# Optimization experiments

Measured on AMD Instinct MI355X. Metric: run time of the kernel, lower is better.

Reference implementation:

```python
import jax, jax.numpy as jnp
import numpy as np

C_IN = 1024
N_HEADS = 16
C_HEAD = C_IN // N_HEADS  # 64
ROPE_BASE = 10000.0


def setup_inputs() -> dict:
    key = jax.random.key(0)
    ks = jax.random.split(key, 7)
    B, S = 2, 2048
    q = jax.random.normal(ks[0], (B, S, C_IN), dtype=jnp.float32)
    k = jax.random.normal(ks[1], (B, S, C_IN), dtype=jnp.float32)
    v = jax.random.normal(ks[2], (B, S, C_IN), dtype=jnp.float32)
    # nn.Linear weights [out, in], y = x @ W.T (no bias)
    sc = 1.0 / np.sqrt(C_IN)
    Wq = jax.random.uniform(ks[3], (C_IN, C_IN), jnp.float32, -sc, sc)
    Wk = jax.random.uniform(ks[4], (C_IN, C_IN), jnp.float32, -sc, sc)
    Wv = jax.random.uniform(ks[5], (C_IN, C_IN), jnp.float32, -sc, sc)
    Wo = jax.random.uniform(ks[6], (C_IN, C_IN), jnp.float32, -sc, sc)
    return {"q": q, "k": k, "v": v, "Wq": Wq, "Wk": Wk, "Wv": Wv, "Wo": Wo}


def _rope_tables(S, dtype):
    inv_freq = 1.0 / (ROPE_BASE ** (jnp.arange(0, C_HEAD, 2, dtype=jnp.float32) / C_HEAD))
    t = jnp.arange(S, dtype=jnp.float32)
    freqs = jnp.einsum('i,j->ij', t, inv_freq)          # [S, C_HEAD/2]
    emb = jnp.concatenate([freqs, freqs], axis=-1)      # [S, C_HEAD]
    cos = jnp.cos(emb)[None, None, :, :].astype(dtype)  # [1,1,S,D]
    sin = jnp.sin(emb)[None, None, :, :].astype(dtype)
    return cos, sin


def _rotate_half(x):
    x1, x2 = jnp.split(x, 2, axis=-1)
    return jnp.concatenate([-x2, x1], axis=-1)


def reference(q, k, v, Wq, Wk, Wv, Wo):
    B, S, _ = q.shape
    # QKV projections, reshape to [B, H, S, D]
    def proj(x, W):
        return (x @ W.T).reshape(B, -1, N_HEADS, C_HEAD).transpose(0, 2, 1, 3)
    qh, kh, vh = proj(q, Wq), proj(k, Wk), proj(v, Wv)
    # rotary embedding
    cos, sin = _rope_tables(S, qh.dtype)
    qh = qh * cos + _rotate_half(qh) * sin
    kh = kh * cos + _rotate_half(kh) * sin
    # scaled dot-product attention (no mask, dropout p=0)
    scale = 1.0 / np.sqrt(C_HEAD)
    scores = jnp.einsum('bhqd,bhkd->bhqk', qh, kh) * scale
    attn = jax.nn.softmax(scores, axis=-1)              # [B,H,S,S]
    out = jnp.einsum('bhqk,bhkd->bhqd', attn, vh)
    out = out.transpose(0, 2, 1, 3).reshape(B, S, N_HEADS * C_HEAD)
    out = out @ Wo.T
    return out, attn
```

## Files before the change

### kernel.cpp

```cpp
#include <hip/hip_runtime.h>
#include <cmath>

typedef __bf16 bhalf;
typedef __bf16 bf16x4 __attribute__((ext_vector_type(4)));
typedef __bf16 bf16x8 __attribute__((ext_vector_type(8)));
typedef float f32x4 __attribute__((ext_vector_type(4)));

#define MFMA16(a, b, c) __builtin_amdgcn_mfma_f32_16x16x32_bf16(a, b, c, 0, 0, 0)

namespace {
constexpr int Bn = 2, Sn = 2048, Cn = 1024, Hn = 16, Dn = 64;
constexpr int Zn = Bn * Hn;
constexpr int Mn = Bn * Sn;
}

__device__ __forceinline__ void cvt_hilo8(const float4& v0, const float4& v1,
                                          bf16x8& hi, bf16x8& lo) {
  float f[8] = {v0.x, v0.y, v0.z, v0.w, v1.x, v1.y, v1.z, v1.w};
#pragma unroll
  for (int i = 0; i < 8; ++i) {
    bhalf h = (bhalf)f[i];
    hi[i] = h;
    lo[i] = (bhalf)(f[i] - (float)h);
  }
}

template <int MODE, bool A_BF16>
__global__ __launch_bounds__(256) void proj_mfma(
    const void* __restrict__ Av, const void* __restrict__ AvLo,
    const float* __restrict__ W, float* __restrict__ out_f32,
    bhalf* __restrict__ dst_hi, bhalf* __restrict__ dst_lo) {
  __shared__ bhalf BsH[64][40];
  __shared__ bhalf BsL[64][40];
  const int tid = threadIdx.x;
  const int lane = tid & 63, w = tid >> 6;
  const int l15 = lane & 15, lg = lane >> 4;
  const int nB = blockIdx.x << 6, mB = blockIdx.y << 6;
  const int row = mB + w * 16 + l15;
  f32x4 acc[4] = {};

  const int sr = tid >> 2, sc = (tid & 3) << 3;
  for (int k0 = 0; k0 < Cn; k0 += 32) {
    {
      const float* wp = W + (size_t)(nB + sr) * Cn + k0 + sc;
      float4 w0 = *(const float4*)wp;
      float4 w1 = *(const float4*)(wp + 4);
      bf16x8 h, l;
      cvt_hilo8(w0, w1, h, l);
      *(bf16x8*)&BsH[sr][sc] = h;
      *(bf16x8*)&BsL[sr][sc] = l;
    }
    __syncthreads();
    bf16x8 aH, aL;
    if constexpr (A_BF16) {
      aH = *(const bf16x8*)((const bhalf*)Av + (size_t)row * Cn + k0 + lg * 8);
      aL = *(const bf16x8*)((const bhalf*)AvLo + (size_t)row * Cn + k0 + lg * 8);
    } else {
      const float* A = (const float*)Av;
      float4 a0 = *(const float4*)(A + (size_t)row * Cn + k0 + lg * 8);
      float4 a1 = *(const float4*)(A + (size_t)row * Cn + k0 + lg * 8 + 4);
      cvt_hilo8(a0, a1, aH, aL);
    }
#pragma unroll
    for (int j = 0; j < 4; ++j) {
      bf16x8 bH = *(const bf16x8*)&BsH[16 * j + l15][lg * 8];
      bf16x8 bL = *(const bf16x8*)&BsL[16 * j + l15][lg * 8];
      acc[j] = MFMA16(aH, bH, acc[j]);
      acc[j] = MFMA16(aH, bL, acc[j]);
      acc[j] = MFMA16(aL, bH, acc[j]);
    }
    __syncthreads();
  }

  const int mRow = mB + w * 16 + lg * 4;
  if constexpr (MODE == 0) {
#pragma unroll
    for (int j = 0; j < 4; ++j) {
      const int n = nB + 16 * j + l15;
#pragma unroll
      for (int r = 0; r < 4; ++r)
        out_f32[(size_t)(mRow + r) * Cn + n] = acc[j][r];
    }
  } else if constexpr (MODE == 1) {
    const int hh = nB >> 6;
#pragma unroll
    for (int jj = 0; jj < 2; ++jj) {
      const int d1 = 16 * jj + l15;
      const float invf = 1.0f / powf(10000.0f, (float)d1 * (1.0f / 32.0f));
#pragma unroll
      for (int r = 0; r < 4; ++r) {
        const int m = mRow + r;
        const int b = m >> 11, s = m & (Sn - 1);
        float sn, cs;
        sincosf((float)s * invf, &sn, &cs);
        const float y1 = acc[jj][r], y2 = acc[jj + 2][r];
        const float o1 = y1 * cs - y2 * sn;
        const float o2 = y2 * cs + y1 * sn;
        const size_t base = (((size_t)(b * Hn + hh)) * Sn + s) * Dn;
        bhalf h1 = (bhalf)o1, h2 = (bhalf)o2;
        dst_hi[base + d1] = h1;
        dst_lo[base + d1] = (bhalf)(o1 - (float)h1);
        dst_hi[base + d1 + 32] = h2;
        dst_lo[base + d1 + 32] = (bhalf)(o2 - (float)h2);
      }
    }
  } else {
    const int hh = nB >> 6;
#pragma unroll
    for (int j = 0; j < 4; ++j) {
      const int d = 16 * j + l15;
#pragma unroll
      for (int r = 0; r < 4; ++r) {
        const int m = mRow + r;
        const int b = m >> 11, s = m & (Sn - 1);
        dst_hi[(((size_t)(b * Hn + hh)) * Dn + d) * Sn + s] = (bhalf)acc[j][r];
      }
    }
  }
}

__device__ __forceinline__ void load_q(const bhalf* __restrict__ qhH,
                                       const bhalf* __restrict__ qhL,
                                       size_t zrow, int sBt, int l15, int lg,
                                       bf16x8 (&qH)[2][2], bf16x8 (&qL)[2][2]) {
#pragma unroll
  for (int qf = 0; qf < 2; ++qf)
#pragma unroll
    for (int sl = 0; sl < 2; ++sl) {
      const size_t off = (zrow + sBt + qf * 16 + l15) * Dn + sl * 32 + lg * 8;
      qH[qf][sl] = *(const bf16x8*)(qhH + off);
      qL[qf][sl] = *(const bf16x8*)(qhL + off);
    }
}

__global__ __launch_bounds__(256) void attn_fused(
    const bhalf* __restrict__ qhH, const bhalf* __restrict__ qhL,
    const bhalf* __restrict__ khH, const bhalf* __restrict__ khL,
    const bhalf* __restrict__ vt, float* __restrict__ attn,
    bhalf* __restrict__ ctxH, bhalf* __restrict__ ctxL) {
  __shared__ float pt[4][32][36];
  __shared__ float lsum[4][32];
  __shared__ float linv[32];

  const int tid = threadIdx.x, lane = tid & 63, w = tid >> 6;
  const int l15 = lane & 15, lg = lane >> 4;
  const int gx = blockIdx.x;
  const int z = gx & 31;
  const int gq = gx >> 5;
  const int sB0 = gq << 7;
  const int bb = z >> 4, hh = z & 15;
  const size_t zrow = (size_t)z * Sn;
  const size_t kRow = zrow * Dn;
  const int kw = w << 9;

  bf16x8 qHc[2][2], qLc[2][2], qHp[2][2], qLp[2][2];
  load_q(qhH, qhL, zrow, sB0, l15, lg, qHc, qLc);

  float invqB[2] = {0.f, 0.f};
  f32x4 acc[2][4];

  for (int tau = 0; tau <= 4; ++tau) {
    const bool hasA = (tau < 4), hasB = (tau > 0);
    const int sBb = sB0 + ((tau - 1) << 5);
    float sum0 = 0.f, sum1 = 0.f;
    if (hasB) {
#pragma unroll
      for (int qf = 0; qf < 2; ++qf)
#pragma unroll
        for (int g = 0; g < 4; ++g) acc[qf][g] = f32x4{0.f, 0.f, 0.f, 0.f};
    }

    for (int cc = 0; cc < 8; ++cc) {
      const int kb0 = kw + (cc << 6);
#pragma unroll
      for (int ch = 0; ch < 2; ++ch) {
        const int kbc = kb0 + (ch << 5);
#pragma unroll
        for (int t2 = 0; t2 < 2; ++t2) {
          const int kb = kbc + (t2 << 4);
          const bhalf* kp = khH + kRow + (size_t)(kb + l15) * Dn + lg * 8;
          const bhalf* kq = khL + kRow + (size_t)(kb + l15) * Dn + lg * 8;
          bf16x8 kH0 = *(const bf16x8*)kp, kH1 = *(const bf16x8*)(kp + 32);
          bf16x8 kL0 = *(const bf16x8*)kq, kL1 = *(const bf16x8*)(kq + 32);
          if (hasA) {
#pragma unroll
            for (int qf = 0; qf < 2; ++qf) {
              f32x4 cA = {}, cB = {};
              cA = MFMA16(kH0, qHc[qf][0], cA); cA = MFMA16(kH1, qHc[qf][1], cA);
              cB = MFMA16(kL0, qHc[qf][0], cB); cB = MFMA16(kL1, qHc[qf][1], cB);
              cA = MFMA16(kH0, qLc[qf][0], cA); cA = MFMA16(kH1, qLc[qf][1], cA);
              f32x4 c = cA + cB;
              float s = __expf(c[0] * 0.125f) + __expf(c[1] * 0.125f) +
                        __expf(c[2] * 0.125f) + __expf(c[3] * 0.125f);
              if (qf == 0) sum0 += s; else sum1 += s;
            }
          }
          if (hasB) {
#pragma unroll
            for (int qf = 0; qf < 2; ++qf) {
              f32x4 cA = {}, cB = {};
              cA = MFMA16(kH0, qHp[qf][0], cA); cA = MFMA16(kH1, qHp[qf][1], cA);
              cB = MFMA16(kL0, qHp[qf][0], cB); cB = MFMA16(kL1, qHp[qf][1], cB);
              cA = MFMA16(kH0, qLp[qf][0], cA); cA = MFMA16(kH1, qLp[qf][1], cA);
              f32x4 c = cA + cB;
              f32x4 p;
#pragma unroll
              for (int r = 0; r < 4; ++r)
                p[r] = __expf(c[r] * 0.125f) * invqB[qf];
              *(f32x4*)&pt[w][qf * 16 + l15][(t2 << 4) + (lg << 2)] = p;
            }
          }
        }
        if (hasB) {
          const int srow = lane >> 3, scol = (lane & 7) << 2;
#pragma unroll
          for (int s = 0; s < 4; ++s) {
            const int row = (s << 3) + srow;
            f32x4 vv = *(const f32x4*)&pt[w][row][scol];
            __builtin_nontemporal_store(
                vv, (f32x4*)(attn + (zrow + sBb + row) * Sn + kbc + scol));
          }
#pragma unroll
          for (int qf = 0; qf < 2; ++qf) {
            f32x4 pa = *(const f32x4*)&pt[w][qf * 16 + l15][lg << 3];
            f32x4 pc = *(const f32x4*)&pt[w][qf * 16 + l15][(lg << 3) + 4];
            bf16x8 pbv;
#pragma unroll
            for (int e = 0; e < 4; ++e) {
              pbv[e] = (bhalf)pa[e];
              pbv[4 + e] = (bhalf)pc[e];
            }
#pragma unroll
            for (int g = 0; g < 4; ++g) {
              const bf16x8 va = *(const bf16x8*)(
                  vt + ((size_t)z * Dn + g * 16 + l15) * Sn + kbc + lg * 8);
              acc[qf][g] = MFMA16(va, pbv, acc[qf][g]);
            }
          }
        }
      }
    }

    if (hasA) {
      sum0 += __shfl_xor(sum0, 16); sum0 += __shfl_xor(sum0, 32);
      sum1 += __shfl_xor(sum1, 16); sum1 += __shfl_xor(sum1, 32);
      if (lane < 16) {
        lsum[w][l15] = sum0;
        lsum[w][16 + l15] = sum1;
      }
    }
    __syncthreads();
    if (hasA && tid < 32)
      linv[tid] =
          1.0f / (lsum[0][tid] + lsum[1][tid] + lsum[2][tid] + lsum[3][tid]);
    if (hasB) {
      float* fb = (float*)&pt[w][0][0];
      float* fb0 = (float*)&pt[0][0][0];
      float* fb1 = (float*)&pt[1][0][0];
      float* fb2 = (float*)&pt[2][0][0];
      float* fb3 = (float*)&pt[3][0][0];
#pragma unroll
      for (int qf = 0; qf < 2; ++qf) {
#pragma unroll
        for (int g = 0; g < 4; ++g)
#pragma unroll
          for (int r = 0; r < 4; ++r)
            fb[l15 * 72 + g * 16 + lg * 4 + r] = acc[qf][g][r];
        __syncthreads();
        {
          const int qq = tid >> 4, d4 = (tid & 15) << 2;
          f32x4 rs = *(const f32x4*)&fb0[qq * 72 + d4];
          rs += *(const f32x4*)&fb1[qq * 72 + d4];
          rs += *(const f32x4*)&fb2[qq * 72 + d4];
          rs += *(const f32x4*)&fb3[qq * 72 + d4];
          const size_t off =
              ((size_t)bb * Sn + sBb + qf * 16 + qq) * Cn + hh * Dn + d4;
          bf16x4 hv, lv;
#pragma unroll
          for (int e = 0; e < 4; ++e) {
            bhalf h = (bhalf)rs[e];
            hv[e] = h;
            lv[e] = (bhalf)(rs[e] - (float)h);
          }
          *(bf16x4*)(ctxH + off) = hv;
          *(bf16x4*)(ctxL + off) = lv;
        }
        __syncthreads();
      }
    } else {
      __syncthreads();
    }
    if (hasA) {
      invqB[0] = linv[l15];
      invqB[1] = linv[16 + l15];
#pragma unroll
      for (int qf = 0; qf < 2; ++qf)
#pragma unroll
        for (int sl = 0; sl < 2; ++sl) {
          qHp[qf][sl] = qHc[qf][sl];
          qLp[qf][sl] = qLc[qf][sl];
        }
      if (tau < 3)
        load_q(qhH, qhL, zrow, sB0 + ((tau + 1) << 5), l15, lg, qHc, qLc);
    }
  }
}

extern "C" void kernel_launch(void* const* d_in, const int* in_sizes, int n_in,
                              void* d_out, int out_size, void* d_ws, size_t ws_size,
                              hipStream_t stream) {
  const float* q = (const float*)d_in[0];
  const float* k = (const float*)d_in[1];
  const float* v = (const float*)d_in[2];
  const float* Wq = (const float*)d_in[3];
  const float* Wk = (const float*)d_in[4];
  const float* Wv = (const float*)d_in[5];
  const float* Wo = (const float*)d_in[6];

  float* out = (float*)d_out;
  float* attn = out + (size_t)Mn * Cn;
  bhalf* vt = (bhalf*)d_out;

  bhalf* qhH = (bhalf*)d_ws;
  bhalf* qhL = qhH + (size_t)Mn * Cn;
  bhalf* khH = qhL + (size_t)Mn * Cn;
  bhalf* khL = khH + (size_t)Mn * Cn;
  bhalf* ctxH = khL + (size_t)Mn * Cn;
  bhalf* ctxL = ctxH + (size_t)Mn * Cn;

  dim3 gP(Cn / 64, Mn / 64);
  proj_mfma<1, false><<<gP, 256, 0, stream>>>(q, nullptr, Wq, nullptr, qhH, qhL);
  proj_mfma<1, false><<<gP, 256, 0, stream>>>(k, nullptr, Wk, nullptr, khH, khL);
  proj_mfma<2, false><<<gP, 256, 0, stream>>>(v, nullptr, Wv, nullptr, vt, nullptr);

  attn_fused<<<Zn * (Sn / 128), 256, 0, stream>>>(qhH, qhL, khH, khL, vt, attn,
                                                  ctxH, ctxL);

  proj_mfma<0, true><<<gP, 256, 0, stream>>>(ctxH, ctxL, Wo, out, nullptr, nullptr);
}
```

Before: 435.1 us.

## Split fused attention into separate row-sum and write kernels with finer grids

Replaces the software-pipelined fused attention kernel, which looped over four 32-row query tiles per block, with two kernels. The first computes softmax denominators and stores their inverses in a scratch area inside the output buffer. The second recomputes the scores, writes normalized attention and accumulates P·V. Each kernel launches four times as many blocks, one 32-row tile each, to raise parallelism and drop the pipelining register pressure, at the cost of an extra launch and a global round trip for the inverse sums.

```diff
diff --git a/kernel.cpp b/kernel.cpp
--- a/kernel.cpp
+++ b/kernel.cpp
@@ -133,176 +133,161 @@
     }
 }
 
-__global__ __launch_bounds__(256) void attn_fused(
+__global__ __launch_bounds__(256) void attn_sums(
     const bhalf* __restrict__ qhH, const bhalf* __restrict__ qhL,
     const bhalf* __restrict__ khH, const bhalf* __restrict__ khL,
-    const bhalf* __restrict__ vt, float* __restrict__ attn,
-    bhalf* __restrict__ ctxH, bhalf* __restrict__ ctxL) {
-  __shared__ float pt[4][32][36];
+    float* __restrict__ linv_g) {
   __shared__ float lsum[4][32];
-  __shared__ float linv[32];
-
   const int tid = threadIdx.x, lane = tid & 63, w = tid >> 6;
   const int l15 = lane & 15, lg = lane >> 4;
   const int gx = blockIdx.x;
   const int z = gx & 31;
-  const int gq = gx >> 5;
-  const int sB0 = gq << 7;
+  const int sB = (gx >> 5) << 5;
+  const size_t zrow = (size_t)z * Sn;
+  const size_t kRow = zrow * Dn;
+  const int kw = w << 9;
+
+  bf16x8 qH[2][2], qL[2][2];
+  load_q(qhH, qhL, zrow, sB, l15, lg, qH, qL);
+
+  float sum0 = 0.f, sum1 = 0.f;
+  for (int cc = 0; cc < 32; ++cc) {
+    const int kb = kw + (cc << 4);
+    const bhalf* kp = khH + kRow + (size_t)(kb + l15) * Dn + lg * 8;
+    const bhalf* kq = khL + kRow + (size_t)(kb + l15) * Dn + lg * 8;
+    bf16x8 kH0 = *(const bf16x8*)kp, kH1 = *(const bf16x8*)(kp + 32);
+    bf16x8 kL0 = *(const bf16x8*)kq, kL1 = *(const bf16x8*)(kq + 32);
+#pragma unroll
+    for (int qf = 0; qf < 2; ++qf) {
+      f32x4 cA = {}, cB = {};
+      cA = MFMA16(kH0, qH[qf][0], cA); cA = MFMA16(kH1, qH[qf][1], cA);
+      cB = MFMA16(kL0, qH[qf][0], cB); cB = MFMA16(kL1, qH[qf][1], cB);
+      cA = MFMA16(kH0, qL[qf][0], cA); cA = MFMA16(kH1, qL[qf][1], cA);
+      f32x4 c = cA + cB;
+      float s = __expf(c[0] * 0.125f) + __expf(c[1] * 0.125f) +
+                __expf(c[2] * 0.125f) + __expf(c[3] * 0.125f);
+      if (qf == 0) sum0 += s; else sum1 += s;
+    }
+  }
+  sum0 += __shfl_xor(sum0, 16); sum0 += __shfl_xor(sum0, 32);
+  sum1 += __shfl_xor(sum1, 16); sum1 += __shfl_xor(sum1, 32);
+  if (lane < 16) {
+    lsum[w][l15] = sum0;
+    lsum[w][16 + l15] = sum1;
+  }
+  __syncthreads();
+  if (tid < 32)
+    linv_g[zrow + sB + tid] =
+        1.0f / (lsum[0][tid] + lsum[1][tid] + lsum[2][tid] + lsum[3][tid]);
+}
+
+__global__ __launch_bounds__(256) void attn_write(
+    const bhalf* __restrict__ qhH, const bhalf* __restrict__ qhL,
+    const bhalf* __restrict__ khH, const bhalf* __restrict__ khL,
+    const bhalf* __restrict__ vt, const float* __restrict__ linv_g,
+    float* __restrict__ attn, bhalf* __restrict__ ctxH,
+    bhalf* __restrict__ ctxL) {
+  __shared__ float pt[4][32][36];
+  const int tid = threadIdx.x, lane = tid & 63, w = tid >> 6;
+  const int l15 = lane & 15, lg = lane >> 4;
+  const int gx = blockIdx.x;
+  const int z = gx & 31;
+  const int sB = (gx >> 5) << 5;
   const int bb = z >> 4, hh = z & 15;
   const size_t zrow = (size_t)z * Sn;
   const size_t kRow = zrow * Dn;
   const int kw = w << 9;
 
-  bf16x8 qHc[2][2], qLc[2][2], qHp[2][2], qLp[2][2];
-  load_q(qhH, qhL, zrow, sB0, l15, lg, qHc, qLc);
-
-  float invqB[2] = {0.f, 0.f};
-  f32x4 acc[2][4];
-
-  for (int tau = 0; tau <= 4; ++tau) {
-    const bool hasA = (tau < 4), hasB = (tau > 0);
-    const int sBb = sB0 + ((tau - 1) << 5);
-    float sum0 = 0.f, sum1 = 0.f;
-    if (hasB) {
-#pragma unroll
-      for (int qf = 0; qf < 2; ++qf)
-#pragma unroll
-        for (int g = 0; g < 4; ++g) acc[qf][g] = f32x4{0.f, 0.f, 0.f, 0.f};
-    }
-
-    for (int cc = 0; cc < 8; ++cc) {
-      const int kb0 = kw + (cc << 6);
-#pragma unroll
-      for (int ch = 0; ch < 2; ++ch) {
-        const int kbc = kb0 + (ch << 5);
-#pragma unroll
-        for (int t2 = 0; t2 < 2; ++t2) {
-          const int kb = kbc + (t2 << 4);
-          const bhalf* kp = khH + kRow + (size_t)(kb + l15) * Dn + lg * 8;
-          const bhalf* kq = khL + kRow + (size_t)(kb + l15) * Dn + lg * 8;
-          bf16x8 kH0 = *(const bf16x8*)kp, kH1 = *(const bf16x8*)(kp + 32);
-          bf16x8 kL0 = *(const bf16x8*)kq, kL1 = *(const bf16x8*)(kq + 32);
-          if (hasA) {
-#pragma unroll
-            for (int qf = 0; qf < 2; ++qf) {
-              f32x4 cA = {}, cB = {};
-              cA = MFMA16(kH0, qHc[qf][0], cA); cA = MFMA16(kH1, qHc[qf][1], cA);
-              cB = MFMA16(kL0, qHc[qf][0], cB); cB = MFMA16(kL1, qHc[qf][1], cB);
-              cA = MFMA16(kH0, qLc[qf][0], cA); cA = MFMA16(kH1, qLc[qf][1], cA);
-              f32x4 c = cA + cB;
-              float s = __expf(c[0] * 0.125f) + __expf(c[1] * 0.125f) +
-                        __expf(c[2] * 0.125f) + __expf(c[3] * 0.125f);
-              if (qf == 0) sum0 += s; else sum1 += s;
-            }
-          }
-          if (hasB) {
-#pragma unroll
-            for (int qf = 0; qf < 2; ++qf) {
-              f32x4 cA = {}, cB = {};
-              cA = MFMA16(kH0, qHp[qf][0], cA); cA = MFMA16(kH1, qHp[qf][1], cA);
-              cB = MFMA16(kL0, qHp[qf][0], cB); cB = MFMA16(kL1, qHp[qf][1], cB);
-              cA = MFMA16(kH0, qLp[qf][0], cA); cA = MFMA16(kH1, qLp[qf][1], cA);
-              f32x4 c = cA + cB;
-              f32x4 p;
-#pragma unroll
-              for (int r = 0; r < 4; ++r)
-                p[r] = __expf(c[r] * 0.125f) * invqB[qf];
-              *(f32x4*)&pt[w][qf * 16 + l15][(t2 << 4) + (lg << 2)] = p;
-            }
-          }
-        }
-        if (hasB) {
-          const int srow = lane >> 3, scol = (lane & 7) << 2;
-#pragma unroll
-          for (int s = 0; s < 4; ++s) {
-            const int row = (s << 3) + srow;
-            f32x4 vv = *(const f32x4*)&pt[w][row][scol];
-            __builtin_nontemporal_store(
-                vv, (f32x4*)(attn + (zrow + sBb + row) * Sn + kbc + scol));
-          }
-#pragma unroll
-          for (int qf = 0; qf < 2; ++qf) {
-            f32x4 pa = *(const f32x4*)&pt[w][qf * 16 + l15][lg << 3];
-            f32x4 pc = *(const f32x4*)&pt[w][qf * 16 + l15][(lg << 3) + 4];
-            bf16x8 pbv;
-#pragma unroll
-            for (int e = 0; e < 4; ++e) {
-              pbv[e] = (bhalf)pa[e];
-              pbv[4 + e] = (bhalf)pc[e];
-            }
-#pragma unroll
-            for (int g = 0; g < 4; ++g) {
-              const bf16x8 va = *(const bf16x8*)(
-                  vt + ((size_t)z * Dn + g * 16 + l15) * Sn + kbc + lg * 8);
-              acc[qf][g] = MFMA16(va, pbv, acc[qf][g]);
-            }
-          }
-        }
-      }
-    }
-
-    if (hasA) {
-      sum0 += __shfl_xor(sum0, 16); sum0 += __shfl_xor(sum0, 32);
-      sum1 += __shfl_xor(sum1, 16); sum1 += __shfl_xor(sum1, 32);
-      if (lane < 16) {
-        lsum[w][l15] = sum0;
-        lsum[w][16 + l15] = sum1;
-      }
-    }
+  bf16x8 qH[2][2], qL[2][2];
+  load_q(qhH, qhL, zrow, sB, l15, lg, qH, qL);
+  const float invq[2] = {linv_g[zrow + sB + l15], linv_g[zrow + sB + 16 + l15]};
+
+  f32x4 acc[2][4] = {};
+
+  for (int cc = 0; cc < 16; ++cc) {
+    const int kbc = kw + (cc << 5);
+#pragma unroll
+    for (int t2 = 0; t2 < 2; ++t2) {
+      const int kb = kbc + (t2 << 4);
+      const bhalf* kp = khH + kRow + (size_t)(kb + l15) * Dn + lg * 8;
+      const bhalf* kq = khL + kRow + (size_t)(kb + l15) * Dn + lg * 8;
+      bf16x8 kH0 = *(const bf16x8*)kp, kH1 = *(const bf16x8*)(kp + 32);
+      bf16x8 kL0 = *(const bf16x8*)kq, kL1 = *(const bf16x8*)(kq + 32);
+#pragma unroll
+      for (int qf = 0; qf < 2; ++qf) {
+        f32x4 cA = {}, cB = {};
+        cA = MFMA16(kH0, qH[qf][0], cA); cA = MFMA16(kH1, qH[qf][1], cA);
+        cB = MFMA16(kL0, qH[qf][0], cB); cB = MFMA16(kL1, qH[qf][1], cB);
+        cA = MFMA16(kH0, qL[qf][0], cA); cA = MFMA16(kH1, qL[qf][1], cA);
+        f32x4 c = cA + cB;
+        f32x4 p;
+#pragma unroll
+        for (int r = 0; r < 4; ++r) p[r] = __expf(c[r] * 0.125f) * invq[qf];
+        *(f32x4*)&pt[w][qf * 16 + l15][(t2 << 4) + (lg << 2)] = p;
+      }
+    }
+    {
+      const int srow = lane >> 3, scol = (lane & 7) << 2;
+#pragma unroll
+      for (int s = 0; s < 4; ++s) {
+        const int row = (s << 3) + srow;
+        f32x4 vv = *(const f32x4*)&pt[w][row][scol];
+        __builtin_nontemporal_store(
+            vv, (f32x4*)(attn + (zrow + sB + row) * Sn + kbc + scol));
+      }
+    }
+#pragma unroll
+    for (int qf = 0; qf < 2; ++qf) {
+      f32x4 pa = *(const f32x4*)&pt[w][qf * 16 + l15][lg << 3];
+      f32x4 pc = *(const f32x4*)&pt[w][qf * 16 + l15][(lg << 3) + 4];
+      bf16x8 pbv;
+#pragma unroll
+      for (int e = 0; e < 4; ++e) {
+        pbv[e] = (bhalf)pa[e];
+        pbv[4 + e] = (bhalf)pc[e];
+      }
+#pragma unroll
+      for (int g = 0; g < 4; ++g) {
+        const bf16x8 va = *(const bf16x8*)(
+            vt + ((size_t)z * Dn + g * 16 + l15) * Sn + kbc + lg * 8);
+        acc[qf][g] = MFMA16(va, pbv, acc[qf][g]);
+      }
+    }
+  }
+
+  __syncthreads();
+  float* fb = (float*)&pt[w][0][0];
+  float* fb0 = (float*)&pt[0][0][0];
+  float* fb1 = (float*)&pt[1][0][0];
+  float* fb2 = (float*)&pt[2][0][0];
+  float* fb3 = (float*)&pt[3][0][0];
+#pragma unroll
+  for (int qf = 0; qf < 2; ++qf) {
+#pragma unroll
+    for (int g = 0; g < 4; ++g)
+#pragma unroll
+      for (int r = 0; r < 4; ++r)
+        fb[l15 * 72 + g * 16 + lg * 4 + r] = acc[qf][g][r];
     __syncthreads();
-    if (hasA && tid < 32)
-      linv[tid] =
-          1.0f / (lsum[0][tid] + lsum[1][tid] + lsum[2][tid] + lsum[3][tid]);
-    if (hasB) {
-      float* fb = (float*)&pt[w][0][0];
-      float* fb0 = (float*)&pt[0][0][0];
-      float* fb1 = (float*)&pt[1][0][0];
-      float* fb2 = (float*)&pt[2][0][0];
-      float* fb3 = (float*)&pt[3][0][0];
-#pragma unroll
-      for (int qf = 0; qf < 2; ++qf) {
-#pragma unroll
-        for (int g = 0; g < 4; ++g)
-#pragma unroll
-          for (int r = 0; r < 4; ++r)
-            fb[l15 * 72 + g * 16 + lg * 4 + r] = acc[qf][g][r];
-        __syncthreads();
-        {
-          const int qq = tid >> 4, d4 = (tid & 15) << 2;
-          f32x4 rs = *(const f32x4*)&fb0[qq * 72 + d4];
-          rs += *(const f32x4*)&fb1[qq * 72 + d4];
-          rs += *(const f32x4*)&fb2[qq * 72 + d4];
-          rs += *(const f32x4*)&fb3[qq * 72 + d4];
-          const size_t off =
-              ((size_t)bb * Sn + sBb + qf * 16 + qq) * Cn + hh * Dn + d4;
-          bf16x4 hv, lv;
-#pragma unroll
-          for (int e = 0; e < 4; ++e) {
-            bhalf h = (bhalf)rs[e];
-            hv[e] = h;
-            lv[e] = (bhalf)(rs[e] - (float)h);
-          }
-          *(bf16x4*)(ctxH + off) = hv;
-          *(bf16x4*)(ctxL + off) = lv;
-        }
-        __syncthreads();
-      }
-    } else {
-      __syncthreads();
-    }
-    if (hasA) {
-      invqB[0] = linv[l15];
-      invqB[1] = linv[16 + l15];
-#pragma unroll
-      for (int qf = 0; qf < 2; ++qf)
-#pragma unroll
-        for (int sl = 0; sl < 2; ++sl) {
-          qHp[qf][sl] = qHc[qf][sl];
-          qLp[qf][sl] = qLc[qf][sl];
-        }
-      if (tau < 3)
-        load_q(qhH, qhL, zrow, sB0 + ((tau + 1) << 5), l15, lg, qHc, qLc);
-    }
+    {
+      const int qq = tid >> 4, d4 = (tid & 15) << 2;
+      f32x4 rs = *(const f32x4*)&fb0[qq * 72 + d4];
+      rs += *(const f32x4*)&fb1[qq * 72 + d4];
+      rs += *(const f32x4*)&fb2[qq * 72 + d4];
+      rs += *(const f32x4*)&fb3[qq * 72 + d4];
+      const size_t off =
+          ((size_t)bb * Sn + sB + qf * 16 + qq) * Cn + hh * Dn + d4;
+      bf16x4 hv, lv;
+#pragma unroll
+      for (int e = 0; e < 4; ++e) {
+        bhalf h = (bhalf)rs[e];
+        hv[e] = h;
+        lv[e] = (bhalf)(rs[e] - (float)h);
+      }
+      *(bf16x4*)(ctxH + off) = hv;
+      *(bf16x4*)(ctxL + off) = lv;
+    }
+    __syncthreads();
   }
 }
 
@@ -320,6 +305,7 @@
   float* out = (float*)d_out;
   float* attn = out + (size_t)Mn * Cn;
   bhalf* vt = (bhalf*)d_out;
+  float* linv_g = out + (size_t)Mn * Cn / 2;
 
   bhalf* qhH = (bhalf*)d_ws;
   bhalf* qhL = qhH + (size_t)Mn * Cn;
@@ -331,10 +317,13 @@
   dim3 gP(Cn / 64, Mn / 64);
   proj_mfma<1, false><<<gP, 256, 0, stream>>>(q, nullptr, Wq, nullptr, qhH, qhL);
   proj_mfma<1, false><<<gP, 256, 0, stream>>>(k, nullptr, Wk, nullptr, khH, khL);
+
+  attn_sums<<<Zn * (Sn / 32), 256, 0, stream>>>(qhH, qhL, khH, khL, linv_g);
+
   proj_mfma<2, false><<<gP, 256, 0, stream>>>(v, nullptr, Wv, nullptr, vt, nullptr);
 
-  attn_fused<<<Zn * (Sn / 128), 256, 0, stream>>>(qhH, qhL, khH, khL, vt, attn,
-                                                  ctxH, ctxL);
+  attn_write<<<Zn * (Sn / 32), 256, 0, stream>>>(qhH, qhL, khH, khL, vt, linv_g,
+                                                 attn, ctxH, ctxL);
 
   proj_mfma<0, true><<<gP, 256, 0, stream>>>(ctxH, ctxL, Wo, out, nullptr, nullptr);
 }
```

Result: slower. 536.2 us (+23.2%).
